# Kernel optimization log

Measured on AMD Instinct MI355X. Metric: run time of the kernel, lower is better.

## Reference

```python
import jax, jax.numpy as jnp
import numpy as np

NB_KNN = 10
T = 0.07
NUM_CLASSES = 50
EPS = 1e-12  # torch F.normalize eps


def _l2norm(x, axis):
    n = jnp.sqrt(jnp.sum(x * x, axis=axis, keepdims=True))
    return x / jnp.maximum(n, EPS)


def setup_inputs() -> dict:
    key = jax.random.key(0)
    k1, k2, k3 = jax.random.split(key, 3)
    B, N, D = 1024, 200000, 256
    test_features = jax.random.normal(k1, (B, D), dtype=jnp.float32)
    train_features = jax.random.normal(k2, (N, D), dtype=jnp.float32)
    train_labels = jax.random.randint(k3, (N,), 0, NUM_CLASSES, dtype=jnp.int64)
    return {
        "test_features": test_features,
        "train_features": train_features,
        "train_labels": train_labels,
    }


def reference(test_features, train_features, train_labels):
    # Faithful to torch: normalize(train_features.T, dim=1) -> normalize [D, N]
    # along axis 1 (the N axis), exactly as the original module does.
    gallery = _l2norm(train_features.T, axis=1)          # [D, N]
    q = _l2norm(test_features, axis=1)                   # [B, D]
    sim = q @ gallery                                    # [B, N]
    topk_sims, idx = jax.lax.top_k(sim, NB_KNN)          # [B, k], [B, k]
    neighbors_labels = train_labels[idx]                 # [B, k]
    w = jax.nn.softmax(topk_sims / T, axis=1)            # [B, k]
    # one-hot weighted scatter-sum into class scores
    onehot = jax.nn.one_hot(neighbors_labels, NUM_CLASSES, dtype=w.dtype)  # [B, k, C]
    return jnp.sum(onehot * w[:, :, None], axis=1)       # [B, C]
```

## Files before the change

kernel.cpp:

```cpp
#include <hip/hip_runtime.h>
#include <hip/hip_bf16.h>
#include <math.h>
#include <stdint.h>

#define DDIM 256
#define CAP  320
#define NCLS 50

typedef short bf16x8_t __attribute__((ext_vector_type(8)));
typedef float f32x4_t  __attribute__((ext_vector_type(4)));

__device__ __forceinline__ void gl_lds16(const void* g, void* l) {
  __builtin_amdgcn_global_load_lds(
      (__attribute__((address_space(1))) unsigned int*)(uintptr_t)g,
      (__attribute__((address_space(3))) unsigned int*)l,
      16, 0, 0);
}

__device__ __forceinline__ unsigned short bf16bits(float v) {
  __hip_bfloat16 h = __float2bfloat16(v);
  return *reinterpret_cast<unsigned short*>(&h);
}

__global__ void k_cast_colsq(const float* __restrict__ train,
                             __hip_bfloat16* __restrict__ tbf,
                             double* __restrict__ colsq, int N) {
  const int t = threadIdx.x;
  const int rsub = t >> 6;
  const int c4 = (t & 63) * 4;
  const int nb = gridDim.x;
  int per = (N + nb - 1) / nb; per = (per + 3) & ~3;
  const int r0 = blockIdx.x * per;
  int r1 = r0 + per; if (r1 > N) r1 = N;
  double a0 = 0, a1 = 0, a2 = 0, a3 = 0;
  for (int r = r0 + rsub; r < r1; r += 4) {
    float4 v = *(const float4*)(train + (size_t)r * DDIM + c4);
    if (tbf) {
      ushort4 u;
      u.x = bf16bits(v.x); u.y = bf16bits(v.y);
      u.z = bf16bits(v.z); u.w = bf16bits(v.w);
      *(ushort4*)(tbf + (size_t)r * DDIM + c4) = u;
    }
    a0 = fma((double)v.x, (double)v.x, a0);
    a1 = fma((double)v.y, (double)v.y, a1);
    a2 = fma((double)v.z, (double)v.z, a2);
    a3 = fma((double)v.w, (double)v.w, a3);
  }
  __shared__ double red[4][DDIM];
  red[rsub][c4 + 0] = a0; red[rsub][c4 + 1] = a1;
  red[rsub][c4 + 2] = a2; red[rsub][c4 + 3] = a3;
  __syncthreads();
  double s = red[0][t] + red[1][t] + red[2][t] + red[3][t];
  atomicAdd(&colsq[t], s);
}

__global__ void k_prep(const float* __restrict__ test, const double* __restrict__ colsq,
                       float* __restrict__ qs, __hip_bfloat16* __restrict__ qs_bf,
                       float* __restrict__ tau, int B) {
  const int row = blockIdx.x, t = threadIdx.x;
  const int wid = t >> 6, lane = t & 63;
  __shared__ float ps[4];
  __shared__ float stot;
  float v = test[(size_t)row * DDIM + t];
  float ss = v * v;
#pragma unroll
  for (int o = 32; o > 0; o >>= 1) ss += __shfl_down(ss, o, 64);
  if (lane == 0) ps[wid] = ss;
  __syncthreads();
  if (t == 0) stot = ps[0] + ps[1] + ps[2] + ps[3];
  __syncthreads();
  float rn   = fmaxf(sqrtf(stot), 1e-12f);
  float coln = fmaxf(sqrtf((float)colsq[t]), 1e-12f);
  float qv   = (v / rn) / coln;
  qs[(size_t)row * DDIM + t] = qv;
  qs_bf[(size_t)row * DDIM + t] = __float2bfloat16(qv);
  float s2 = qv * qv;
#pragma unroll
  for (int o = 32; o > 0; o >>= 1) s2 += __shfl_down(s2, o, 64);
  if (lane == 0) ps[wid] = s2;
  __syncthreads();
  if (t == 0) tau[row] = 3.30f * sqrtf(ps[0] + ps[1] + ps[2] + ps[3]);
}

__global__ __launch_bounds__(256, 2)
void k_mfma(const __hip_bfloat16* __restrict__ qs_bf,
            const __hip_bfloat16* __restrict__ train_bf,
            const float* __restrict__ tau, int* __restrict__ cidx,
            int* __restrict__ cnt, int N, int B) {
  __shared__ __align__(16) char Bsh[65536];
  __shared__ float tau_s[1024];
  const int tid = threadIdx.x;
  const int w = tid >> 6, lane = tid & 63;
  const int l15 = lane & 15, l4 = lane >> 4;
  const int col0 = blockIdx.x * 128;

#pragma unroll
  for (int i = 0; i < 16; ++i) {
    const int idx = w * 16 + i;
    const int s = idx >> 3, g = idx & 7;
    int c = col0 + g * 16 + l15; if (c >= N) c = N - 1;
    gl_lds16(train_bf + (size_t)c * DDIM + s * 32 + l4 * 8, Bsh + idx * 1024);
  }
  for (int i = tid; i < 1024; i += 256) {
    int rr = i; if (rr >= B) rr = B - 1;
    tau_s[i] = tau[rr];
  }
  __syncthreads();

  const int npan = (B + 127) / 128;
  bf16x8_t afc[2], afn[2];
  {
    int r0 = w * 32 + l15;      if (r0 >= B) r0 = B - 1;
    int r1 = w * 32 + 16 + l15; if (r1 >= B) r1 = B - 1;
    afc[0] = *(const bf16x8_t*)(qs_bf + (size_t)r0 * DDIM + l4 * 8);
    afc[1] = *(const bf16x8_t*)(qs_bf + (size_t)r1 * DDIM + l4 * 8);
  }

  for (int p = 0; p < npan; ++p) {
    f32x4_t acc[2][8];
#pragma unroll
    for (int m = 0; m < 2; ++m)
#pragma unroll
      for (int n = 0; n < 8; ++n) acc[m][n] = (f32x4_t){0.f, 0.f, 0.f, 0.f};

#pragma unroll
    for (int s = 0; s < 8; ++s) {
      const int sp1 = (s + 1) & 7;
      const int pn = (s == 7) ? (p + 1 < npan ? p + 1 : p) : p;
      {
        int r0 = pn * 128 + w * 32 + l15;      if (r0 >= B) r0 = B - 1;
        int r1 = pn * 128 + w * 32 + 16 + l15; if (r1 >= B) r1 = B - 1;
        const size_t ko = (size_t)sp1 * 32 + l4 * 8;
        afn[0] = *(const bf16x8_t*)(qs_bf + (size_t)r0 * DDIM + ko);
        afn[1] = *(const bf16x8_t*)(qs_bf + (size_t)r1 * DDIM + ko);
      }
#pragma unroll
      for (int n = 0; n < 8; ++n) {
        bf16x8_t bf = *(const bf16x8_t*)(Bsh + (s * 8 + n) * 1024 + lane * 16);
        acc[0][n] = __builtin_amdgcn_mfma_f32_16x16x32_bf16(afc[0], bf, acc[0][n], 0, 0, 0);
        acc[1][n] = __builtin_amdgcn_mfma_f32_16x16x32_bf16(afc[1], bf, acc[1][n], 0, 0, 0);
      }
      afc[0] = afn[0]; afc[1] = afn[1];
    }

#pragma unroll
    for (int m = 0; m < 2; ++m) {
#pragma unroll
      for (int n = 0; n < 8; ++n) {
        const int coln = col0 + n * 16 + l15;
        if (coln < N) {
#pragma unroll
          for (int r = 0; r < 4; ++r) {
            const int rl = p * 128 + w * 32 + m * 16 + l4 * 4 + r;
            if (rl < B && acc[m][n][r] > tau_s[rl]) {
              int pos = atomicAdd(&cnt[rl], 1);
              if (pos < CAP) cidx[(size_t)rl * CAP + pos] = coln;
            }
          }
        }
      }
    }
  }
}

#define DOT4(ACC, A, Bv)                                                     \
  ACC = fmaf((A).x, (Bv).x, ACC); ACC = fmaf((A).y, (Bv).y, ACC);            \
  ACC = fmaf((A).z, (Bv).z, ACC); ACC = fmaf((A).w, (Bv).w, ACC);

__global__ __launch_bounds__(256, 4)
void k_gemm(const float* __restrict__ train, const float* __restrict__ qs,
            const float* __restrict__ tau, int* __restrict__ cidx,
            int* __restrict__ cnt, int N, int B, int tpc) {
  __shared__ float4 As4[8 * 128];
  __shared__ float4 Bs4[8 * 64];
  const int tid = threadIdx.x;
  const int tx = tid & 15, ty = tid >> 4;
  const int wid = tid >> 6, lane = tid & 63;
  const int row0 = blockIdx.y * 128;
  const int colbase = blockIdx.x * tpc * 64;
  float tau_r[8];
#pragma unroll
  for (int i = 0; i < 8; ++i) {
    int r = row0 + ty + 16 * i; if (r >= B) r = B - 1;
    tau_r[i] = tau[r];
  }
  int rL = row0 + lane;      if (rL >= B) rL = B - 1;
  int rH = row0 + 64 + lane; if (rH >= B) rH = B - 1;
  const float* aptrL = qs + (size_t)rL * DDIM;
  const float* aptrH = qs + (size_t)rH * DDIM;
  for (int tile = 0; tile < tpc; ++tile) {
    const int col0 = colbase + tile * 64;
    if (col0 >= N) break;
    int bcol = col0 + lane; if (bcol >= N) bcol = N - 1;
    const float* bptr = train + (size_t)bcol * DDIM;
    float acc[8][4];
#pragma unroll
    for (int i = 0; i < 8; ++i)
#pragma unroll
      for (int j = 0; j < 4; ++j) acc[i][j] = 0.f;
    for (int s = 0; s < 8; ++s) {
      const int kk0 = s * 32;
      __syncthreads();
#pragma unroll
      for (int j = 0; j < 4; ++j) {
        const int slot = wid + 4 * j;
        const int m = slot >> 1, half = slot & 1;
        gl_lds16((half ? aptrH : aptrL) + kk0 + 4 * m, &As4[m * 128 + half * 64]);
      }
#pragma unroll
      for (int j = 0; j < 2; ++j) {
        const int m = wid + 4 * j;
        gl_lds16(bptr + kk0 + 4 * m, &Bs4[m * 64]);
      }
      __syncthreads();
#pragma unroll
      for (int k4 = 0; k4 < 8; ++k4) {
        float4 a[8], b[4];
#pragma unroll
        for (int i = 0; i < 8; ++i) a[i] = As4[k4 * 128 + ty + 16 * i];
#pragma unroll
        for (int j = 0; j < 4; ++j) b[j] = Bs4[k4 * 64 + tx + 16 * j];
#pragma unroll
        for (int i = 0; i < 8; ++i)
#pragma unroll
          for (int j = 0; j < 4; ++j) { DOT4(acc[i][j], a[i], b[j]) }
      }
    }
#pragma unroll
    for (int i = 0; i < 8; ++i) {
      const int r = row0 + ty + 16 * i;
#pragma unroll
      for (int j = 0; j < 4; ++j) {
        const int c = col0 + tx + 16 * j;
        if (acc[i][j] > tau_r[i] && c < N && r < B) {
          int p = atomicAdd(&cnt[r], 1);
          if (p < CAP) cidx[(size_t)r * CAP + p] = c;
        }
      }
    }
  }
}

__global__ void k_fallback(const float* __restrict__ train, const float* __restrict__ qs,
                           int* __restrict__ cidx, int* __restrict__ cnt, int N) {
  const int row = blockIdx.x;
  const int t = threadIdx.x;
  const int c0 = cnt[row];
  if (c0 >= 10 && c0 <= CAP) return;
  __shared__ float q[DDIM];
  if (t < DDIM) q[t] = qs[(size_t)row * DDIM + t];
  __syncthreads();
  float lv[10]; int li[10];
#pragma unroll
  for (int k = 0; k < 10; ++k) { lv[k] = -INFINITY; li[k] = 0x7FFFFFFF; }
  for (int c = t; c < N; c += 256) {
    const float* tr = train + (size_t)c * DDIM;
    float s = 0.f;
    for (int d = 0; d < DDIM; ++d) s = fmaf(q[d], tr[d], s);
    if (s > lv[9]) {
      int p = 9;
      while (p > 0 && s > lv[p - 1]) { lv[p] = lv[p - 1]; li[p] = li[p - 1]; --p; }
      lv[p] = s; li[p] = c;
    }
  }
  __shared__ float rv[256]; __shared__ int ri[256]; __shared__ int rt_[256];
  __shared__ int topi[10];
  int pt = 0;
  for (int k = 0; k < 10; ++k) {
    rv[t] = (pt < 10) ? lv[pt] : -INFINITY;
    ri[t] = (pt < 10) ? li[pt] : 0x7FFFFFFF;
    rt_[t] = t;
    __syncthreads();
    for (int s2 = 128; s2 > 0; s2 >>= 1) {
      if (t < s2) {
        float ov = rv[t + s2]; int oi = ri[t + s2];
        if (ov > rv[t] || (ov == rv[t] && oi < ri[t])) {
          rv[t] = ov; ri[t] = oi; rt_[t] = rt_[t + s2];
        }
      }
      __syncthreads();
    }
    const int win = rt_[0];
    if (t == 0) topi[k] = ri[0];
    __syncthreads();
    if (t == win) ++pt;
  }
  if (t < 10) cidx[(size_t)row * CAP + t] = topi[t];
  if (t == 0) cnt[row] = 10;
}

__global__ void k_rescore(const float* __restrict__ train, const float* __restrict__ qs,
                          const int* __restrict__ cidx, const int* __restrict__ cnt,
                          double* __restrict__ dval) {
  const int row = blockIdx.x;
  const int t = threadIdx.x, wid = t >> 6, lane = t & 63;
  __shared__ float qsh[DDIM];
  if (t < DDIM) qsh[t] = qs[(size_t)row * DDIM + t];
  __syncthreads();
  int n = cnt[row]; if (n > CAP) n = CAP;
  for (int ci = wid; ci < n; ci += 4) {
    const int c = cidx[(size_t)row * CAP + ci];
    const float4 tv = *(const float4*)(train + (size_t)c * DDIM + lane * 4);
    const float4 qv = *(const float4*)(qsh + lane * 4);
    double s = (double)tv.x * qv.x + (double)tv.y * qv.y +
               (double)tv.z * qv.z + (double)tv.w * qv.w;
#pragma unroll
    for (int o = 32; o > 0; o >>= 1) s += __shfl_down(s, o, 64);
    if (lane == 0) dval[(size_t)row * CAP + ci] = s;
  }
}

__global__ void k_finalize(const double* __restrict__ dval, const int* __restrict__ cidx,
                           const int* __restrict__ cnt, const int* __restrict__ labels,
                           float* __restrict__ out) {
  const int row = blockIdx.x;
  const int t = threadIdx.x;
  int n = cnt[row]; if (n > CAP) n = CAP;
  __shared__ double sv[CAP]; __shared__ int si[CAP];
  for (int i = t; i < CAP; i += 256) {
    sv[i] = (i < n) ? dval[(size_t)row * CAP + i] : -INFINITY;
    si[i] = (i < n) ? cidx[(size_t)row * CAP + i] : 0x7FFFFFFF;
  }
  __syncthreads();
  __shared__ double rv[256]; __shared__ int ri[256]; __shared__ int rp[256];
  __shared__ double topv[10]; __shared__ int topl[10];
  __shared__ int wpos;
  for (int k = 0; k < 10; ++k) {
    double bv = sv[t]; int bi = si[t]; int bp = t;
    if (t + 256 < CAP) {
      double v2 = sv[t + 256]; int i2 = si[t + 256];
      if (v2 > bv || (v2 == bv && i2 < bi)) { bv = v2; bi = i2; bp = t + 256; }
    }
    rv[t] = bv; ri[t] = bi; rp[t] = bp;
    __syncthreads();
    for (int s2 = 128; s2 > 0; s2 >>= 1) {
      if (t < s2) {
        double ov = rv[t + s2]; int oi = ri[t + s2];
        if (ov > rv[t] || (ov == rv[t] && oi < ri[t])) {
          rv[t] = ov; ri[t] = oi; rp[t] = rp[t + s2];
        }
      }
      __syncthreads();
    }
    if (t == 0) { topv[k] = rv[0]; topl[k] = ri[0]; wpos = rp[0]; }
    __syncthreads();
    if (t == 0) sv[wpos] = -INFINITY;
    __syncthreads();
  }
  __shared__ double oc[NCLS];
  if (t < NCLS) oc[t] = 0.0;
  __syncthreads();
  if (t == 0) {
    const double m = topv[0];
    double w[10]; double ssum = 0.0;
#pragma unroll
    for (int k = 0; k < 10; ++k) { w[k] = exp((topv[k] - m) / 0.07); ssum += w[k]; }
#pragma unroll
    for (int k = 0; k < 10; ++k) oc[labels[topl[k]]] += w[k] / ssum;
  }
  __syncthreads();
  if (t < NCLS) out[(size_t)row * NCLS + t] = (float)oc[t];
}

extern "C" void kernel_launch(void* const* d_in, const int* in_sizes, int n_in,
                              void* d_out, int out_size, void* d_ws, size_t ws_size,
                              hipStream_t stream) {
  const float* test   = (const float*)d_in[0];
  const float* train  = (const float*)d_in[1];
  const int*   labels = (const int*)d_in[2];
  float* out = (float*)d_out;
  const int B = in_sizes[0] / DDIM;
  const int N = in_sizes[2];
  (void)n_in; (void)out_size;

  char* w = (char*)d_ws;
  size_t off = 0;
  auto alloc = [&](size_t bytes) {
    size_t o = off; off = (off + bytes + 255) & ~(size_t)255; return o;
  };
  double* colsq = (double*)(w + alloc(2048));
  int*    cnt   = (int*)(w + alloc((size_t)B * 4));
  float*  tau   = (float*)(w + alloc((size_t)B * 4));
  float*  qs    = (float*)(w + alloc((size_t)B * DDIM * 4));
  __hip_bfloat16* qs_bf = (__hip_bfloat16*)(w + alloc((size_t)B * DDIM * 2));
  int*    cidx  = (int*)(w + alloc((size_t)B * CAP * 4));
  double* dval  = (double*)(w + alloc((size_t)B * CAP * 8));
  __hip_bfloat16* train_bf = (__hip_bfloat16*)(w + alloc((size_t)N * DDIM * 2));
  const bool use_mfma = (ws_size >= off);

  hipMemsetAsync(d_ws, 0, 2048 + (size_t)B * 4, stream);

  if (use_mfma) {
    hipLaunchKernelGGL(k_cast_colsq, dim3(512), dim3(256), 0, stream,
                       train, train_bf, colsq, N);
    hipLaunchKernelGGL(k_prep, dim3(B), dim3(256), 0, stream,
                       test, colsq, qs, qs_bf, tau, B);
    hipLaunchKernelGGL(k_mfma, dim3((N + 127) / 128), dim3(256), 0, stream,
                       qs_bf, train_bf, tau, cidx, cnt, N, B);
  } else {
    hipLaunchKernelGGL(k_cast_colsq, dim3(512), dim3(256), 0, stream,
                       train, (__hip_bfloat16*)nullptr, colsq, N);
    hipLaunchKernelGGL(k_prep, dim3(B), dim3(256), 0, stream,
                       test, colsq, qs, qs_bf, tau, B);
    const int CT = (N + 63) / 64;
    const int rb = (B + 127) / 128;
    int bx = 2048 / (rb > 0 ? rb : 1); if (bx < 1) bx = 1;
    int tpc = (CT + bx - 1) / bx;
    int chunks = (CT + tpc - 1) / tpc;
    hipLaunchKernelGGL(k_gemm, dim3(chunks, rb), dim3(256), 0, stream,
                       train, qs, tau, cidx, cnt, N, B, tpc);
  }

  hipLaunchKernelGGL(k_fallback, dim3(B), dim3(256), 0, stream,
                     train, qs, cidx, cnt, N);
  hipLaunchKernelGGL(k_rescore,  dim3(B), dim3(256), 0, stream,
                     train, qs, cidx, cnt, dval);
  hipLaunchKernelGGL(k_finalize, dim3(B), dim3(256), 0, stream,
                     dval, cidx, cnt, labels, out);
}
```

Before: 661.5 us.

## Fuse fallback, rescore and finalize into one tail kernel; preload A fragments

```diff
diff --git a/kernel.cpp b/kernel.cpp
--- a/kernel.cpp
+++ b/kernel.cpp
@@ -108,15 +108,18 @@
   __syncthreads();
 
   const int npan = (B + 127) / 128;
-  bf16x8_t afc[2], afn[2];
-  {
-    int r0 = w * 32 + l15;      if (r0 >= B) r0 = B - 1;
-    int r1 = w * 32 + 16 + l15; if (r1 >= B) r1 = B - 1;
-    afc[0] = *(const bf16x8_t*)(qs_bf + (size_t)r0 * DDIM + l4 * 8);
-    afc[1] = *(const bf16x8_t*)(qs_bf + (size_t)r1 * DDIM + l4 * 8);
-  }
-
   for (int p = 0; p < npan; ++p) {
+    int r0 = p * 128 + w * 32 + l15;      if (r0 >= B) r0 = B - 1;
+    int r1 = p * 128 + w * 32 + 16 + l15; if (r1 >= B) r1 = B - 1;
+    const __hip_bfloat16* a0 = qs_bf + (size_t)r0 * DDIM + l4 * 8;
+    const __hip_bfloat16* a1 = qs_bf + (size_t)r1 * DDIM + l4 * 8;
+    bf16x8_t ap[8][2];
+#pragma unroll
+    for (int s = 0; s < 8; ++s) {
+      ap[s][0] = *(const bf16x8_t*)(a0 + s * 32);
+      ap[s][1] = *(const bf16x8_t*)(a1 + s * 32);
+    }
+
     f32x4_t acc[2][8];
 #pragma unroll
     for (int m = 0; m < 2; ++m)
@@ -125,22 +128,15 @@
 
 #pragma unroll
     for (int s = 0; s < 8; ++s) {
-      const int sp1 = (s + 1) & 7;
-      const int pn = (s == 7) ? (p + 1 < npan ? p + 1 : p) : p;
-      {
-        int r0 = pn * 128 + w * 32 + l15;      if (r0 >= B) r0 = B - 1;
-        int r1 = pn * 128 + w * 32 + 16 + l15; if (r1 >= B) r1 = B - 1;
-        const size_t ko = (size_t)sp1 * 32 + l4 * 8;
-        afn[0] = *(const bf16x8_t*)(qs_bf + (size_t)r0 * DDIM + ko);
-        afn[1] = *(const bf16x8_t*)(qs_bf + (size_t)r1 * DDIM + ko);
-      }
+      bf16x8_t bfr[8];
+#pragma unroll
+      for (int n = 0; n < 8; ++n)
+        bfr[n] = *(const bf16x8_t*)(Bsh + (s * 8 + n) * 1024 + lane * 16);
 #pragma unroll
       for (int n = 0; n < 8; ++n) {
-        bf16x8_t bf = *(const bf16x8_t*)(Bsh + (s * 8 + n) * 1024 + lane * 16);
-        acc[0][n] = __builtin_amdgcn_mfma_f32_16x16x32_bf16(afc[0], bf, acc[0][n], 0, 0, 0);
-        acc[1][n] = __builtin_amdgcn_mfma_f32_16x16x32_bf16(afc[1], bf, acc[1][n], 0, 0, 0);
-      }
-      afc[0] = afn[0]; afc[1] = afn[1];
+        acc[0][n] = __builtin_amdgcn_mfma_f32_16x16x32_bf16(ap[s][0], bfr[n], acc[0][n], 0, 0, 0);
+        acc[1][n] = __builtin_amdgcn_mfma_f32_16x16x32_bf16(ap[s][1], bfr[n], acc[1][n], 0, 0, 0);
+      }
     }
 
 #pragma unroll
@@ -241,88 +237,77 @@
   }
 }
 
-__global__ void k_fallback(const float* __restrict__ train, const float* __restrict__ qs,
-                           int* __restrict__ cidx, int* __restrict__ cnt, int N) {
+__global__ void k_tail(const float* __restrict__ train, const float* __restrict__ qs,
+                       const int* __restrict__ cidx, const int* __restrict__ cnt,
+                       const int* __restrict__ labels, float* __restrict__ out, int N) {
   const int row = blockIdx.x;
   const int t = threadIdx.x;
-  const int c0 = cnt[row];
-  if (c0 >= 10 && c0 <= CAP) return;
-  __shared__ float q[DDIM];
-  if (t < DDIM) q[t] = qs[(size_t)row * DDIM + t];
-  __syncthreads();
-  float lv[10]; int li[10];
-#pragma unroll
-  for (int k = 0; k < 10; ++k) { lv[k] = -INFINITY; li[k] = 0x7FFFFFFF; }
-  for (int c = t; c < N; c += 256) {
-    const float* tr = train + (size_t)c * DDIM;
-    float s = 0.f;
-    for (int d = 0; d < DDIM; ++d) s = fmaf(q[d], tr[d], s);
-    if (s > lv[9]) {
-      int p = 9;
-      while (p > 0 && s > lv[p - 1]) { lv[p] = lv[p - 1]; li[p] = li[p - 1]; --p; }
-      lv[p] = s; li[p] = c;
-    }
-  }
-  __shared__ float rv[256]; __shared__ int ri[256]; __shared__ int rt_[256];
-  __shared__ int topi[10];
-  int pt = 0;
-  for (int k = 0; k < 10; ++k) {
-    rv[t] = (pt < 10) ? lv[pt] : -INFINITY;
-    ri[t] = (pt < 10) ? li[pt] : 0x7FFFFFFF;
-    rt_[t] = t;
+  const int wv = t >> 6, lane = t & 63;
+  __shared__ float qsh[DDIM];
+  __shared__ int si[CAP];
+  __shared__ double sv[CAP];
+  if (t < DDIM) qsh[t] = qs[(size_t)row * DDIM + t];
+  int n = cnt[row];
+  const bool bad = (n < 10 || n > CAP);
+  for (int i = t; i < CAP; i += 256) {
+    si[i] = (!bad && i < n) ? cidx[(size_t)row * CAP + i] : 0x7FFFFFFF;
+    sv[i] = -INFINITY;
+  }
+  __syncthreads();
+
+  if (bad) {
+    float lv[10]; int li[10];
+#pragma unroll
+    for (int k = 0; k < 10; ++k) { lv[k] = -INFINITY; li[k] = 0x7FFFFFFF; }
+    for (int c = t; c < N; c += 256) {
+      const float* tr = train + (size_t)c * DDIM;
+      float s = 0.f;
+      for (int d = 0; d < DDIM; ++d) s = fmaf(qsh[d], tr[d], s);
+      if (s > lv[9]) {
+        int p = 9;
+        while (p > 0 && s > lv[p - 1]) { lv[p] = lv[p - 1]; li[p] = li[p - 1]; --p; }
+        lv[p] = s; li[p] = c;
+      }
+    }
+    __shared__ float rv[256]; __shared__ int ri[256]; __shared__ int rt_[256];
+    int pt = 0;
+    for (int k = 0; k < 10; ++k) {
+      rv[t] = (pt < 10) ? lv[pt] : -INFINITY;
+      ri[t] = (pt < 10) ? li[pt] : 0x7FFFFFFF;
+      rt_[t] = t;
+      __syncthreads();
+      for (int s2 = 128; s2 > 0; s2 >>= 1) {
+        if (t < s2) {
+          float ov = rv[t + s2]; int oi = ri[t + s2];
+          if (ov > rv[t] || (ov == rv[t] && oi < ri[t])) {
+            rv[t] = ov; ri[t] = oi; rt_[t] = rt_[t + s2];
+          }
+        }
+        __syncthreads();
+      }
+      const int win = rt_[0];
+      if (t == 0) si[k] = ri[0];
+      __syncthreads();
+      if (t == win) ++pt;
+    }
+    n = 10;
     __syncthreads();
-    for (int s2 = 128; s2 > 0; s2 >>= 1) {
-      if (t < s2) {
-        float ov = rv[t + s2]; int oi = ri[t + s2];
-        if (ov > rv[t] || (ov == rv[t] && oi < ri[t])) {
-          rv[t] = ov; ri[t] = oi; rt_[t] = rt_[t + s2];
-        }
-      }
-      __syncthreads();
-    }
-    const int win = rt_[0];
-    if (t == 0) topi[k] = ri[0];
-    __syncthreads();
-    if (t == win) ++pt;
-  }
-  if (t < 10) cidx[(size_t)row * CAP + t] = topi[t];
-  if (t == 0) cnt[row] = 10;
-}
-
-__global__ void k_rescore(const float* __restrict__ train, const float* __restrict__ qs,
-                          const int* __restrict__ cidx, const int* __restrict__ cnt,
-                          double* __restrict__ dval) {
-  const int row = blockIdx.x;
-  const int t = threadIdx.x, wid = t >> 6, lane = t & 63;
-  __shared__ float qsh[DDIM];
-  if (t < DDIM) qsh[t] = qs[(size_t)row * DDIM + t];
-  __syncthreads();
-  int n = cnt[row]; if (n > CAP) n = CAP;
-  for (int ci = wid; ci < n; ci += 4) {
-    const int c = cidx[(size_t)row * CAP + ci];
+  }
+  int nn = n; if (nn > CAP) nn = CAP;
+
+  for (int ci = wv; ci < nn; ci += 4) {
+    const int c = si[ci];
     const float4 tv = *(const float4*)(train + (size_t)c * DDIM + lane * 4);
     const float4 qv = *(const float4*)(qsh + lane * 4);
     double s = (double)tv.x * qv.x + (double)tv.y * qv.y +
                (double)tv.z * qv.z + (double)tv.w * qv.w;
 #pragma unroll
     for (int o = 32; o > 0; o >>= 1) s += __shfl_down(s, o, 64);
-    if (lane == 0) dval[(size_t)row * CAP + ci] = s;
-  }
-}
-
-__global__ void k_finalize(const double* __restrict__ dval, const int* __restrict__ cidx,
-                           const int* __restrict__ cnt, const int* __restrict__ labels,
-                           float* __restrict__ out) {
-  const int row = blockIdx.x;
-  const int t = threadIdx.x;
-  int n = cnt[row]; if (n > CAP) n = CAP;
-  __shared__ double sv[CAP]; __shared__ int si[CAP];
-  for (int i = t; i < CAP; i += 256) {
-    sv[i] = (i < n) ? dval[(size_t)row * CAP + i] : -INFINITY;
-    si[i] = (i < n) ? cidx[(size_t)row * CAP + i] : 0x7FFFFFFF;
-  }
-  __syncthreads();
-  __shared__ double rv[256]; __shared__ int ri[256]; __shared__ int rp[256];
+    if (lane == 0) sv[ci] = s;
+  }
+  __syncthreads();
+
+  __shared__ double rv2[256]; __shared__ int ri2[256]; __shared__ int rp2[256];
   __shared__ double topv[10]; __shared__ int topl[10];
   __shared__ int wpos;
   for (int k = 0; k < 10; ++k) {
@@ -331,22 +316,23 @@
       double v2 = sv[t + 256]; int i2 = si[t + 256];
       if (v2 > bv || (v2 == bv && i2 < bi)) { bv = v2; bi = i2; bp = t + 256; }
     }
-    rv[t] = bv; ri[t] = bi; rp[t] = bp;
+    rv2[t] = bv; ri2[t] = bi; rp2[t] = bp;
     __syncthreads();
     for (int s2 = 128; s2 > 0; s2 >>= 1) {
       if (t < s2) {
-        double ov = rv[t + s2]; int oi = ri[t + s2];
-        if (ov > rv[t] || (ov == rv[t] && oi < ri[t])) {
-          rv[t] = ov; ri[t] = oi; rp[t] = rp[t + s2];
+        double ov = rv2[t + s2]; int oi = ri2[t + s2];
+        if (ov > rv2[t] || (ov == rv2[t] && oi < ri2[t])) {
+          rv2[t] = ov; ri2[t] = oi; rp2[t] = rp2[t + s2];
         }
       }
       __syncthreads();
     }
-    if (t == 0) { topv[k] = rv[0]; topl[k] = ri[0]; wpos = rp[0]; }
+    if (t == 0) { topv[k] = rv2[0]; topl[k] = ri2[0]; wpos = rp2[0]; }
     __syncthreads();
     if (t == 0) sv[wpos] = -INFINITY;
     __syncthreads();
   }
+
   __shared__ double oc[NCLS];
   if (t < NCLS) oc[t] = 0.0;
   __syncthreads();
@@ -384,21 +370,20 @@
   float*  qs    = (float*)(w + alloc((size_t)B * DDIM * 4));
   __hip_bfloat16* qs_bf = (__hip_bfloat16*)(w + alloc((size_t)B * DDIM * 2));
   int*    cidx  = (int*)(w + alloc((size_t)B * CAP * 4));
-  double* dval  = (double*)(w + alloc((size_t)B * CAP * 8));
   __hip_bfloat16* train_bf = (__hip_bfloat16*)(w + alloc((size_t)N * DDIM * 2));
   const bool use_mfma = (ws_size >= off);
 
   hipMemsetAsync(d_ws, 0, 2048 + (size_t)B * 4, stream);
 
   if (use_mfma) {
-    hipLaunchKernelGGL(k_cast_colsq, dim3(512), dim3(256), 0, stream,
+    hipLaunchKernelGGL(k_cast_colsq, dim3(1024), dim3(256), 0, stream,
                        train, train_bf, colsq, N);
     hipLaunchKernelGGL(k_prep, dim3(B), dim3(256), 0, stream,
                        test, colsq, qs, qs_bf, tau, B);
     hipLaunchKernelGGL(k_mfma, dim3((N + 127) / 128), dim3(256), 0, stream,
                        qs_bf, train_bf, tau, cidx, cnt, N, B);
   } else {
-    hipLaunchKernelGGL(k_cast_colsq, dim3(512), dim3(256), 0, stream,
+    hipLaunchKernelGGL(k_cast_colsq, dim3(1024), dim3(256), 0, stream,
                        train, (__hip_bfloat16*)nullptr, colsq, N);
     hipLaunchKernelGGL(k_prep, dim3(B), dim3(256), 0, stream,
                        test, colsq, qs, qs_bf, tau, B);
@@ -411,10 +396,6 @@
                        train, qs, tau, cidx, cnt, N, B, tpc);
   }
 
-  hipLaunchKernelGGL(k_fallback, dim3(B), dim3(256), 0, stream,
-                     train, qs, cidx, cnt, N);
-  hipLaunchKernelGGL(k_rescore,  dim3(B), dim3(256), 0, stream,
-                     train, qs, cidx, cnt, dval);
-  hipLaunchKernelGGL(k_finalize, dim3(B), dim3(256), 0, stream,
-                     dval, cidx, cnt, labels, out);
-}
+  hipLaunchKernelGGL(k_tail, dim3(B), dim3(256), 0, stream,
+                     train, qs, cidx, cnt, labels, out, N);
+}
```

Measured after the change: 633.6 us. -4.2%, faster.
